# Performance work log

Measured on AMD Instinct MI355X. Metric: run time of the kernel, lower is better.

Reference implementation:

```python
import jax, jax.numpy as jnp
import numpy as np

NUM_HEADS = 8  # init num_heads


def setup_inputs() -> dict:
    key = jax.random.key(0)
    ks = jax.random.split(key, 8)
    B, N, C, G = 2, 256 * 256, 256, 512  # N hardcoded by original reshape(256*256)
    xq = jax.random.normal(ks[0], (B, N, C), jnp.float32)
    xk = jax.random.normal(ks[1], (B, N, C), jnp.float32)
    xv = jax.random.normal(ks[2], (B, N, C), jnp.float32)
    w_scale = C ** -0.5
    Wq = jax.random.normal(ks[3], (C, C), jnp.float32) * w_scale
    bq = jax.random.normal(ks[4], (C,), jnp.float32) * 0.02
    Wp = jax.random.normal(ks[5], (C, C), jnp.float32) * w_scale
    bp = jax.random.normal(ks[6], (C,), jnp.float32) * 0.02
    # Voronoi cell labels 1..G, each cell exactly N//G tokens, randomly scattered
    # over the 256x256 grid (irregular gather/scatter access, all cells < 1500 tokens).
    labels = jnp.repeat(jnp.arange(1, G + 1, dtype=jnp.int32), N // G)
    Voronoi = jnp.stack([
        jax.random.permutation(jax.random.fold_in(ks[7], b), labels) for b in range(B)
    ]).reshape(B, 256, 256)
    return {"xq": xq, "xk": xk, "xv": xv, "Wq": Wq, "bq": bq,
            "Wp": Wp, "bp": bp, "Voronoi": Voronoi, "num_groups": G}


def reference(xq, xk, xv, Wq, bq, Wp, bp, Voronoi, num_groups):
    B, N, C = xq.shape
    H = NUM_HEADS
    hd = C // H
    scale = hd ** -0.5  # qk_scale default: head_dim ** -0.5
    # NOTE: the original forward projects q, k AND v with self.q (shared weights/bias).
    # This (likely a bug upstream) is preserved faithfully here.
    q = (xq @ Wq.T + bq).reshape(B, N, H, hd)
    k = (xk @ Wq.T + bq).reshape(B, N, H, hd)
    v = (xv @ Wq.T + bq).reshape(B, N, H, hd)
    labels = Voronoi.reshape(B, N)
    order = jnp.argsort(labels, axis=1)   # [B, N] sort tokens by Voronoi cell id
    inv = jnp.argsort(order, axis=1)      # inverse permutation for scatter-back
    S = N // num_groups                   # tokens per cell (static)

    def gather(t):  # [B, N, H, hd] -> [B, G, S, H, hd] grouped by cell
        return jnp.take_along_axis(t, order[:, :, None, None], axis=1).reshape(B, num_groups, S, H, hd)

    qg = gather(q) * scale
    kg = gather(k)
    vg = gather(v)
    attn = jnp.einsum('bgshd,bgthd->bghst', qg, kg)   # per-cell scores [B,G,H,S,S]
    p = jax.nn.softmax(attn, axis=-1)                 # attn_drop=0 (eval)
    og = jnp.einsum('bghst,bgthd->bgshd', p, vg).reshape(B, N, H, hd)
    out = jnp.take_along_axis(og, inv[:, :, None, None], axis=1).reshape(B, N, C)
    return out @ Wp.T + bp                            # proj_drop=0 (eval)
```

## Files before the change

kernel.cpp:

```cpp
#include <hip/hip_runtime.h>
#include <hip/hip_bf16.h>

#define B_    2
#define NTOK  65536
#define C_    256
#define H_    8
#define HD_   32
#define G_    512
#define S_    128
#define BN    (B_*NTOK)
#define M3    (3*BN)

typedef __attribute__((ext_vector_type(8))) short short8;
typedef __attribute__((ext_vector_type(4))) float f32x4;

__device__ __forceinline__ ushort f2bf(float f) {
  __bf16 h = (__bf16)f;
  return __builtin_bit_cast(unsigned short, h);
}
__device__ __forceinline__ unsigned pk2(float lo, float hi) {
  return (unsigned)f2bf(lo) | ((unsigned)f2bf(hi) << 16);
}

__device__ __forceinline__ void gl16(const void* g, void* l) {
  __builtin_amdgcn_global_load_lds(
      (const __attribute__((address_space(1))) unsigned int*)g,
      (__attribute__((address_space(3))) unsigned int*)l, 16, 0, 0);
}

#define SW4(c, r) ((((c) ^ (r) ^ ((r) >> 2))) & 3)
#define SWK32(c, r) ((((c) ^ ((r) >> 1))) & 3)
#define PSL(c, r) ((((c) ^ ((r) & 7) ^ ((((r) >> 3) & 1) << 1))) & 15)
#define VSL(c, ch) ((((c) ^ (((ch) & 7) << 1) ^ (((ch) >> 3) & 3))) & 15)

#define QSCALE 0.25506907131737264f

__global__ __launch_bounds__(256) void k_prep(const float* __restrict__ Wq,
                                              const float* __restrict__ Wp,
                                              ushort* __restrict__ Wq_img,
                                              ushort* __restrict__ Wp_img) {
  int gid = blockIdx.x * 256 + threadIdx.x;
  int w = gid >> 13, rem = gid & 8191;
  if (w == 0) {
    int ks = rem >> 11, rem2 = rem & 2047;
    int r = rem2 >> 3, c = rem2 & 7;
    const float4* s = reinterpret_cast<const float4*>(Wq + (size_t)r * 256 + ks * 64 + c * 8);
    float4 a = s[0], b = s[1];
    uint4 o;
    o.x = pk2(a.x, a.y); o.y = pk2(a.z, a.w);
    o.z = pk2(b.x, b.y); o.w = pk2(b.z, b.w);
    *reinterpret_cast<uint4*>(Wq_img + ks * 16384 + r * 64 + ((c ^ (r & 7)) << 3)) = o;
  } else {
    int h = rem >> 10, r = (rem >> 2) & 255, c = rem & 3;
    const float4* s = reinterpret_cast<const float4*>(Wp + (size_t)r * 256 + h * 32 + c * 8);
    float4 a = s[0], b = s[1];
    uint4 o;
    o.x = pk2(a.x, a.y); o.y = pk2(a.z, a.w);
    o.z = pk2(b.x, b.y); o.w = pk2(b.z, b.w);
    *reinterpret_cast<uint4*>(Wp_img + h * 8192 + r * 32 + (SWK32(c, r) << 3)) = o;
  }
}

__global__ __launch_bounds__(256) void k_group(const int* __restrict__ vor,
                                               int* __restrict__ grp,
                                               int* __restrict__ cnt) {
  int idx = blockIdx.x * 256 + threadIdx.x;
  int b = idx >> 16;
  int n = idx & (NTOK - 1);
  int g = vor[idx] - 1;
  int pos = atomicAdd(&cnt[(b << 9) + g], 1);
  grp[((b << 9) + g) * S_ + pos] = n;
}

__global__ __launch_bounds__(512, 4) void k_proj_qkv(
    const float* __restrict__ xq, const float* __restrict__ xk,
    const float* __restrict__ xv, const ushort* __restrict__ Wq_img,
    const float* __restrict__ bq, ushort* __restrict__ qkv) {
  __shared__ ushort As[128 * 64];
  __shared__ ushort Bs[2][256 * 64];
  int mt = blockIdx.x;
  int t = mt >> 10;
  const float* A = (t == 0) ? xq : (t == 1) ? xk : xv;
  float qsc = (t == 0) ? QSCALE : 1.0f;
  size_t abase = (size_t)(mt & 1023) * 128 * 256;
  int row0 = mt * 128;

  int tid = threadIdx.x, lane = tid & 63, wave = tid >> 6;
  int l15 = lane & 15, hi = lane >> 4;
  int wr = (wave >> 2) * 64, wc = (wave & 3) * 64;
  int sr = tid >> 2, sq = tid & 3;

  const float* aptr = A + abase + (size_t)sr * 256 + sq * 16;
  int boff = wave * 4096 + lane * 16;

  f32x4 acc[4][4] = {};
  float4 ar[2][4];
  {
    const float4* p = reinterpret_cast<const float4*>(aptr);
#pragma unroll
    for (int j = 0; j < 4; ++j) ar[0][j] = p[j];
  }
#pragma unroll
  for (int j = 0; j < 4; ++j)
    gl16((const char*)Wq_img + boff + j * 1024, (char*)Bs[0] + boff + j * 1024);

#pragma unroll
  for (int ks = 0; ks < 4; ++ks) {
    uint4 w0, w1;
    w0.x = pk2(ar[ks & 1][0].x, ar[ks & 1][0].y); w0.y = pk2(ar[ks & 1][0].z, ar[ks & 1][0].w);
    w0.z = pk2(ar[ks & 1][1].x, ar[ks & 1][1].y); w0.w = pk2(ar[ks & 1][1].z, ar[ks & 1][1].w);
    w1.x = pk2(ar[ks & 1][2].x, ar[ks & 1][2].y); w1.y = pk2(ar[ks & 1][2].z, ar[ks & 1][2].w);
    w1.z = pk2(ar[ks & 1][3].x, ar[ks & 1][3].y); w1.w = pk2(ar[ks & 1][3].z, ar[ks & 1][3].w);
    *reinterpret_cast<uint4*>(&As[sr * 64 + (((sq * 2) ^ (sr & 7)) << 3)]) = w0;
    *reinterpret_cast<uint4*>(&As[sr * 64 + (((sq * 2 + 1) ^ (sr & 7)) << 3)]) = w1;
    if (ks < 3) {
      const float4* p = reinterpret_cast<const float4*>(aptr + (ks + 1) * 64);
#pragma unroll
      for (int j = 0; j < 4; ++j) ar[(ks + 1) & 1][j] = p[j];
#pragma unroll
      for (int j = 0; j < 4; ++j)
        gl16((const char*)Wq_img + (ks + 1) * 32768 + boff + j * 1024,
             (char*)Bs[(ks + 1) & 1] + boff + j * 1024);
      asm volatile("s_waitcnt vmcnt(8)" ::: "memory");
    } else {
      asm volatile("s_waitcnt vmcnt(0)" ::: "memory");
    }
    asm volatile("s_waitcnt lgkmcnt(0)" ::: "memory");
    __builtin_amdgcn_s_barrier();
    const ushort* Bcur = Bs[ks & 1];
#pragma unroll
    for (int kk = 0; kk < 2; ++kk) {
      int ck = kk * 4 + hi;
      short8 af[4], bfr[4];
#pragma unroll
      for (int m = 0; m < 4; ++m) {
        int r = wr + m * 16 + l15;
        af[m] = *reinterpret_cast<const short8*>(&As[r * 64 + ((ck ^ (r & 7)) << 3)]);
      }
#pragma unroll
      for (int n = 0; n < 4; ++n) {
        int r = wc + n * 16 + l15;
        bfr[n] = *reinterpret_cast<const short8*>(&Bcur[r * 64 + ((ck ^ (r & 7)) << 3)]);
      }
#pragma unroll
      for (int m = 0; m < 4; ++m)
#pragma unroll
        for (int n = 0; n < 4; ++n)
          acc[m][n] = __builtin_amdgcn_mfma_f32_16x16x32_bf16(af[m], bfr[n], acc[m][n], 0, 0, 0);
    }
    asm volatile("s_waitcnt lgkmcnt(0)" ::: "memory");
    __builtin_amdgcn_s_barrier();
  }

  ushort* Ot = (ushort*)Bs;
#pragma unroll
  for (int n = 0; n < 4; ++n) {
    int col = wc + n * 16 + l15;
    float bv = bq[col];
    int c = col >> 3, ci = col & 7;
#pragma unroll
    for (int m = 0; m < 4; ++m) {
      int r0 = wr + m * 16 + hi * 4;
#pragma unroll
      for (int j = 0; j < 4; ++j) {
        int r = r0 + j;
        int slot = c ^ (((r >> 2) & 3) << 1);
        Ot[r * 256 + slot * 8 + ci] = f2bf((acc[m][n][j] + bv) * qsc);
      }
    }
  }
  __syncthreads();
  {
    size_t gbase = (size_t)row0 * 256;
#pragma unroll
    for (int s = 0; s < 8; ++s) {
      int off = s * 4096 + tid * 8;
      int r = off >> 8, cc = (off >> 3) & 31;
      int slot = cc ^ (((r >> 2) & 3) << 1);
      *reinterpret_cast<uint4*>(qkv + gbase + off) =
          *reinterpret_cast<const uint4*>(Ot + r * 256 + slot * 8);
    }
  }
}

__global__ __launch_bounds__(512) void k_attn_proj(
    const ushort* __restrict__ qkv, const int* __restrict__ grp,
    const ushort* __restrict__ Wp_img, const float* __restrict__ bp,
    float* __restrict__ out) {
  __shared__ int toks[128];
  __shared__ ushort PsB[128 * 128];
  __shared__ ushort Vt[32 * 128];
  __shared__ ushort Oh[128 * 32];
  __shared__ ushort WpS[256 * 32];
  ushort* Qs = PsB;
  ushort* Ks = PsB + 4096;
  ushort* Ps = PsB;

  int bid = blockIdx.x;
  int g = bid & (G_ - 1), b = bid >> 9;
  int tid = threadIdx.x, lane = tid & 63, wave = tid >> 6;
  int l15 = lane & 15, hi = lane >> 4;
  int strip = wave * 16;
  int mg = wave >> 1, ng = wave & 1;

  if (tid < 128) toks[tid] = grp[((b << 9) + g) * S_ + tid];
  __syncthreads();

  int wpoff = wave * 1024 + lane * 16;
  gl16((const char*)Wp_img + wpoff, (char*)WpS + wpoff);
  gl16((const char*)Wp_img + 8192 + wpoff, (char*)WpS + wpoff + 8192);

  f32x4 acc[2][8] = {};

  int r_st = tid >> 2, cp = tid & 3;
  int tok_st = toks[r_st];
  size_t rowq = (size_t)(b * NTOK + tok_st) * 256;
  int chunk_t = r_st >> 3, tl = r_st & 7;

  uint4 qa, ka, va;
  {
    size_t base = rowq + cp * 8;
    qa = *reinterpret_cast<const uint4*>(qkv + base);
    ka = *reinterpret_cast<const uint4*>(qkv + (size_t)BN * 256 + base);
    va = *reinterpret_cast<const uint4*>(qkv + (size_t)2 * BN * 256 + base);
  }

  for (int h = 0; h < 8; ++h) {
    *reinterpret_cast<uint4*>(&Qs[r_st * 32 + SW4(cp, r_st) * 8]) = qa;
    *reinterpret_cast<uint4*>(&Ks[r_st * 32 + SW4(cp, r_st) * 8]) = ka;
    {
      const ushort* pv_ = reinterpret_cast<const ushort*>(&va);
#pragma unroll
      for (int e = 0; e < 8; ++e) {
        int ch = cp * 8 + e;
        Vt[ch * 128 + (VSL(chunk_t, ch) << 3) + tl] = pv_[e];
      }
    }
    asm volatile("s_waitcnt lgkmcnt(0)" ::: "memory");
    __builtin_amdgcn_s_barrier();

    if (h < 7) {
      size_t base = rowq + (h + 1) * 32 + cp * 8;
      qa = *reinterpret_cast<const uint4*>(qkv + base);
      ka = *reinterpret_cast<const uint4*>(qkv + (size_t)BN * 256 + base);
      va = *reinterpret_cast<const uint4*>(qkv + (size_t)2 * BN * 256 + base);
    }

    f32x4 sacc[8] = {};
    {
      int ra = strip + l15;
      short8 aq = *reinterpret_cast<const short8*>(&Qs[ra * 32 + SW4(hi, ra) * 8]);
      short8 bk[8];
#pragma unroll
      for (int n = 0; n < 8; ++n) {
        int r = n * 16 + l15;
        bk[n] = *reinterpret_cast<const short8*>(&Ks[r * 32 + SW4(hi, r) * 8]);
      }
#pragma unroll
      for (int n = 0; n < 8; ++n)
        sacc[n] = __builtin_amdgcn_mfma_f32_16x16x32_bf16(aq, bk[n], sacc[n], 0, 0, 0);
    }
    asm volatile("s_waitcnt lgkmcnt(0)" ::: "memory");
    __builtin_amdgcn_s_barrier();

    float inv[4];
#pragma unroll
    for (int j = 0; j < 4; ++j) {
      float mx = -1e30f;
#pragma unroll
      for (int n = 0; n < 8; ++n) mx = fmaxf(mx, sacc[n][j]);
#pragma unroll
      for (int d = 1; d < 16; d <<= 1) mx = fmaxf(mx, __shfl_xor(mx, d));
      float pv[8], sum = 0.f;
#pragma unroll
      for (int n = 0; n < 8; ++n) { pv[n] = exp2f(sacc[n][j] - mx); sum += pv[n]; }
#pragma unroll
      for (int d = 1; d < 16; d <<= 1) sum += __shfl_xor(sum, d);
      inv[j] = 1.0f / sum;
      int row = strip + hi * 4 + j;
#pragma unroll
      for (int n = 0; n < 8; ++n) {
        int col = n * 16 + l15;
        int chunk = col >> 3;
        Ps[row * 128 + (PSL(chunk, row) << 3) + (col & 7)] = f2bf(pv[n]);
      }
    }
    asm volatile("s_waitcnt lgkmcnt(0)" ::: "memory");

    f32x4 oacc[2] = {};
#pragma unroll
    for (int kk = 0; kk < 4; ++kk) {
      int chunk = kk * 4 + hi;
      int rp = strip + l15;
      short8 pa = *reinterpret_cast<const short8*>(&Ps[rp * 128 + (PSL(chunk, rp) << 3)]);
      short8 bv[2];
#pragma unroll
      for (int n = 0; n < 2; ++n) {
        int ch = n * 16 + l15;
        bv[n] = *reinterpret_cast<const short8*>(&Vt[ch * 128 + (VSL(chunk, ch) << 3)]);
      }
#pragma unroll
      for (int n = 0; n < 2; ++n)
        oacc[n] = __builtin_amdgcn_mfma_f32_16x16x32_bf16(pa, bv[n], oacc[n], 0, 0, 0);
    }
#pragma unroll
    for (int n = 0; n < 2; ++n) {
#pragma unroll
      for (int j = 0; j < 4; ++j) {
        int row = strip + hi * 4 + j;
        int col = n * 16 + l15;
        Oh[row * 32 + (SWK32(col >> 3, row) << 3) + (col & 7)] = f2bf(oacc[n][j] * inv[j]);
      }
    }
    asm volatile("s_waitcnt vmcnt(0)" ::: "memory");
    asm volatile("s_waitcnt lgkmcnt(0)" ::: "memory");
    __builtin_amdgcn_s_barrier();

    {
      short8 af[2], bf[8];
#pragma unroll
      for (int m = 0; m < 2; ++m) {
        int r = mg * 32 + m * 16 + l15;
        af[m] = *reinterpret_cast<const short8*>(&Oh[r * 32 + (SWK32(hi, r) << 3)]);
      }
#pragma unroll
      for (int n = 0; n < 8; ++n) {
        int r = ng * 128 + n * 16 + l15;
        bf[n] = *reinterpret_cast<const short8*>(&WpS[r * 32 + (SWK32(hi, r) << 3)]);
      }
#pragma unroll
      for (int m = 0; m < 2; ++m)
#pragma unroll
        for (int n = 0; n < 8; ++n)
          acc[m][n] = __builtin_amdgcn_mfma_f32_16x16x32_bf16(af[m], bf[n], acc[m][n], 0, 0, 0);
    }
    asm volatile("s_waitcnt lgkmcnt(0)" ::: "memory");
    __builtin_amdgcn_s_barrier();
    if (h < 7) {
      gl16((const char*)Wp_img + (h + 1) * 16384 + wpoff, (char*)WpS + wpoff);
      gl16((const char*)Wp_img + (h + 1) * 16384 + 8192 + wpoff, (char*)WpS + wpoff + 8192);
    }
  }

  float* Of = (float*)PsB;
#pragma unroll
  for (int q = 0; q < 4; ++q) {
    __syncthreads();
    if (mg == q) {
#pragma unroll
      for (int n = 0; n < 8; ++n) {
        int col = ng * 128 + n * 16 + l15;
        float bv = bp[col];
        int c = col >> 2, ci = col & 3;
#pragma unroll
        for (int m = 0; m < 2; ++m) {
#pragma unroll
          for (int j = 0; j < 4; ++j) {
            int lr = m * 16 + hi * 4 + j;
            int slot = c ^ (((lr >> 2) & 3) << 2);
            Of[lr * 256 + slot * 4 + ci] = acc[m][n][j] + bv;
          }
        }
      }
    }
    __syncthreads();
#pragma unroll
    for (int s = 0; s < 4; ++s) {
      int off = s * 2048 + tid * 4;
      int lr = off >> 8, cc = (off >> 2) & 63;
      int slot = cc ^ (((lr >> 2) & 3) << 2);
      int tok = toks[q * 32 + lr];
      *reinterpret_cast<float4*>(out + ((size_t)(b * NTOK + tok)) * 256 + cc * 4) =
          *reinterpret_cast<const float4*>(Of + lr * 256 + slot * 4);
    }
  }
}

extern "C" void kernel_launch(void* const* d_in, const int* in_sizes, int n_in,
                              void* d_out, int out_size, void* d_ws, size_t ws_size,
                              hipStream_t stream) {
  const float* xq = (const float*)d_in[0];
  const float* xk = (const float*)d_in[1];
  const float* xv = (const float*)d_in[2];
  const float* Wq = (const float*)d_in[3];
  const float* bq = (const float*)d_in[4];
  const float* Wp = (const float*)d_in[5];
  const float* bp = (const float*)d_in[6];
  const int*   vor = (const int*)d_in[7];

  char* ws = (char*)d_ws;
  ushort* qkv    = (ushort*)ws;
  int*    grp    = (int*)(ws + (size_t)201326592);
  int*    cnt    = (int*)(ws + (size_t)201850880);
  ushort* Wq_img = (ushort*)(ws + (size_t)201854976);
  ushort* Wp_img = (ushort*)(ws + (size_t)201986048);

  hipMemsetAsync(cnt, 0, B_ * G_ * sizeof(int), stream);
  k_prep<<<dim3(64), dim3(256), 0, stream>>>(Wq, Wp, Wq_img, Wp_img);
  k_group<<<dim3(BN / 256), dim3(256), 0, stream>>>(vor, grp, cnt);
  k_proj_qkv<<<dim3(M3 / 128), dim3(512), 0, stream>>>(xq, xk, xv, Wq_img, bq, qkv);
  k_attn_proj<<<dim3(B_ * G_), dim3(512), 0, stream>>>(qkv, grp, Wp_img, bp, (float*)d_out);
}
```

Measured before the change: 325.3 us.

## Keep softmax probabilities in registers and double-buffer Wp tiles in attention kernel

The attention kernel now computes S^T (K as A operand), so each lane holds a whole score column. Softmax needs only two cross-lane shuffles, and the probabilities are repacked into MFMA A-fragments through lane shuffles instead of going through LDS. This removes the P round-trip through shared memory and one barrier per head. Wp slices are double-buffered and prefetched a head early, which removes the trailing barrier, and the QKV GEMM prefetches its A tiles one step further ahead. The cost is more shuffle instructions and register pressure, and the swizzled fragment layout and vmcnt counts are fragile.

Result: no change. 327.0 us (+0.5%).

```diff
diff --git a/kernel.cpp b/kernel.cpp
--- a/kernel.cpp
+++ b/kernel.cpp
@@ -30,7 +30,6 @@
 
 #define SW4(c, r) ((((c) ^ (r) ^ ((r) >> 2))) & 3)
 #define SWK32(c, r) ((((c) ^ ((r) >> 1))) & 3)
-#define PSL(c, r) ((((c) ^ ((r) & 7) ^ ((((r) >> 3) & 1) << 1))) & 15)
 #define VSL(c, ch) ((((c) ^ (((ch) & 7) << 1) ^ (((ch) >> 3) & 3))) & 15)
 
 #define QSCALE 0.25506907131737264f
@@ -103,6 +102,11 @@
 #pragma unroll
   for (int j = 0; j < 4; ++j)
     gl16((const char*)Wq_img + boff + j * 1024, (char*)Bs[0] + boff + j * 1024);
+  {
+    const float4* p = reinterpret_cast<const float4*>(aptr + 64);
+#pragma unroll
+    for (int j = 0; j < 4; ++j) ar[1][j] = p[j];
+  }
 
 #pragma unroll
   for (int ks = 0; ks < 4; ++ks) {
@@ -114,13 +118,17 @@
     *reinterpret_cast<uint4*>(&As[sr * 64 + (((sq * 2) ^ (sr & 7)) << 3)]) = w0;
     *reinterpret_cast<uint4*>(&As[sr * 64 + (((sq * 2 + 1) ^ (sr & 7)) << 3)]) = w1;
     if (ks < 3) {
-      const float4* p = reinterpret_cast<const float4*>(aptr + (ks + 1) * 64);
-#pragma unroll
-      for (int j = 0; j < 4; ++j) ar[(ks + 1) & 1][j] = p[j];
 #pragma unroll
       for (int j = 0; j < 4; ++j)
         gl16((const char*)Wq_img + (ks + 1) * 32768 + boff + j * 1024,
              (char*)Bs[(ks + 1) & 1] + boff + j * 1024);
+    }
+    if (ks < 2) {
+      const float4* p = reinterpret_cast<const float4*>(aptr + (ks + 2) * 64);
+#pragma unroll
+      for (int j = 0; j < 4; ++j) ar[ks & 1][j] = p[j];
+    }
+    if (ks < 3) {
       asm volatile("s_waitcnt vmcnt(8)" ::: "memory");
     } else {
       asm volatile("s_waitcnt vmcnt(0)" ::: "memory");
@@ -188,13 +196,13 @@
     const ushort* __restrict__ Wp_img, const float* __restrict__ bp,
     float* __restrict__ out) {
   __shared__ int toks[128];
-  __shared__ ushort PsB[128 * 128];
-  __shared__ ushort Vt[32 * 128];
-  __shared__ ushort Oh[128 * 32];
-  __shared__ ushort WpS[256 * 32];
-  ushort* Qs = PsB;
-  ushort* Ks = PsB + 4096;
-  ushort* Ps = PsB;
+  __shared__ ushort shm[32768];
+  ushort* Qs  = shm;
+  ushort* Ks  = shm + 4096;
+  ushort* Vt  = shm + 8192;
+  ushort* Oh  = shm + 12288;
+  ushort* Wp0 = shm + 16384;
+  ushort* Wp1 = shm + 24576;
 
   int bid = blockIdx.x;
   int g = bid & (G_ - 1), b = bid >> 9;
@@ -207,8 +215,8 @@
   __syncthreads();
 
   int wpoff = wave * 1024 + lane * 16;
-  gl16((const char*)Wp_img + wpoff, (char*)WpS + wpoff);
-  gl16((const char*)Wp_img + 8192 + wpoff, (char*)WpS + wpoff + 8192);
+  gl16((const char*)Wp_img + wpoff, (char*)Wp0 + wpoff);
+  gl16((const char*)Wp_img + 8192 + wpoff, (char*)Wp0 + wpoff + 8192);
 
   f32x4 acc[2][8] = {};
 
@@ -226,6 +234,8 @@
   }
 
   for (int h = 0; h < 8; ++h) {
+    ushort* WpCur = (h & 1) ? Wp1 : Wp0;
+    ushort* WpNext = (h & 1) ? Wp0 : Wp1;
     *reinterpret_cast<uint4*>(&Qs[r_st * 32 + SW4(cp, r_st) * 8]) = qa;
     *reinterpret_cast<uint4*>(&Ks[r_st * 32 + SW4(cp, r_st) * 8]) = ka;
     {
@@ -240,6 +250,8 @@
     __builtin_amdgcn_s_barrier();
 
     if (h < 7) {
+      gl16((const char*)Wp_img + (h + 1) * 16384 + wpoff, (char*)WpNext + wpoff);
+      gl16((const char*)Wp_img + (h + 1) * 16384 + 8192 + wpoff, (char*)WpNext + wpoff + 8192);
       size_t base = rowq + (h + 1) * 32 + cp * 8;
       qa = *reinterpret_cast<const uint4*>(qkv + base);
       ka = *reinterpret_cast<const uint4*>(qkv + (size_t)BN * 256 + base);
@@ -249,70 +261,86 @@
     f32x4 sacc[8] = {};
     {
       int ra = strip + l15;
-      short8 aq = *reinterpret_cast<const short8*>(&Qs[ra * 32 + SW4(hi, ra) * 8]);
-      short8 bk[8];
+      short8 qf = *reinterpret_cast<const short8*>(&Qs[ra * 32 + SW4(hi, ra) * 8]);
 #pragma unroll
       for (int n = 0; n < 8; ++n) {
         int r = n * 16 + l15;
-        bk[n] = *reinterpret_cast<const short8*>(&Ks[r * 32 + SW4(hi, r) * 8]);
-      }
-#pragma unroll
-      for (int n = 0; n < 8; ++n)
-        sacc[n] = __builtin_amdgcn_mfma_f32_16x16x32_bf16(aq, bk[n], sacc[n], 0, 0, 0);
-    }
-    asm volatile("s_waitcnt lgkmcnt(0)" ::: "memory");
-    __builtin_amdgcn_s_barrier();
-
-    float inv[4];
-#pragma unroll
-    for (int j = 0; j < 4; ++j) {
-      float mx = -1e30f;
-#pragma unroll
-      for (int n = 0; n < 8; ++n) mx = fmaxf(mx, sacc[n][j]);
-#pragma unroll
-      for (int d = 1; d < 16; d <<= 1) mx = fmaxf(mx, __shfl_xor(mx, d));
-      float pv[8], sum = 0.f;
-#pragma unroll
-      for (int n = 0; n < 8; ++n) { pv[n] = exp2f(sacc[n][j] - mx); sum += pv[n]; }
-#pragma unroll
-      for (int d = 1; d < 16; d <<= 1) sum += __shfl_xor(sum, d);
-      inv[j] = 1.0f / sum;
-      int row = strip + hi * 4 + j;
-#pragma unroll
-      for (int n = 0; n < 8; ++n) {
-        int col = n * 16 + l15;
-        int chunk = col >> 3;
-        Ps[row * 128 + (PSL(chunk, row) << 3) + (col & 7)] = f2bf(pv[n]);
-      }
-    }
-    asm volatile("s_waitcnt lgkmcnt(0)" ::: "memory");
+        short8 kf = *reinterpret_cast<const short8*>(&Ks[r * 32 + SW4(hi, r) * 8]);
+        sacc[n] = __builtin_amdgcn_mfma_f32_16x16x32_bf16(kf, qf, sacc[n], 0, 0, 0);
+      }
+    }
+
+    float mx = -1e30f;
+#pragma unroll
+    for (int n = 0; n < 8; ++n)
+#pragma unroll
+      for (int j = 0; j < 4; ++j) mx = fmaxf(mx, sacc[n][j]);
+    mx = fmaxf(mx, __shfl_xor(mx, 16));
+    mx = fmaxf(mx, __shfl_xor(mx, 32));
+    float p[8][4];
+    float sum = 0.f;
+#pragma unroll
+    for (int n = 0; n < 8; ++n)
+#pragma unroll
+      for (int j = 0; j < 4; ++j) { p[n][j] = exp2f(sacc[n][j] - mx); sum += p[n][j]; }
+    sum += __shfl_xor(sum, 16);
+    sum += __shfl_xor(sum, 32);
+    float inv = 1.0f / sum;
+
+    short8 paf[4];
+#pragma unroll
+    for (int t = 0; t < 4; ++t) {
+      unsigned e0 = pk2(p[2 * t][0], p[2 * t][1]);
+      unsigned e1 = pk2(p[2 * t][2], p[2 * t][3]);
+      unsigned o0 = pk2(p[2 * t + 1][0], p[2 * t + 1][1]);
+      unsigned o1 = pk2(p[2 * t + 1][2], p[2 * t + 1][3]);
+      unsigned pe0 = __shfl_xor(e0, 16), pe1 = __shfl_xor(e1, 16);
+      unsigned po0 = __shfl_xor(o0, 16), po1 = __shfl_xor(o1, 16);
+      bool up = (hi & 1);
+      unsigned E0 = up ? pe0 : e0, E1 = up ? pe1 : e1;
+      unsigned E2 = up ? e0 : pe0, E3 = up ? e1 : pe1;
+      unsigned O0 = up ? po0 : o0, O1 = up ? po1 : o1;
+      unsigned O2 = up ? o0 : po0, O3 = up ? o1 : po1;
+      unsigned s0 = up ? E0 : O0, s1 = up ? E1 : O1;
+      unsigned s2 = up ? E2 : O2, s3 = up ? E3 : O3;
+      unsigned r0 = __shfl_xor(s0, 32), r1 = __shfl_xor(s1, 32);
+      unsigned r2 = __shfl_xor(s2, 32), r3 = __shfl_xor(s3, 32);
+      unsigned f0, f1, f2, f3;
+      if (hi == 0)      { f0 = E0; f1 = E1; f2 = E2; f3 = E3; }
+      else if (hi == 3) { f0 = O0; f1 = O1; f2 = O2; f3 = O3; }
+      else              { f0 = r0; f1 = r1; f2 = r2; f3 = r3; }
+      union { unsigned u[4]; short8 s; } cv;
+      cv.u[0] = f0; cv.u[1] = f1; cv.u[2] = f2; cv.u[3] = f3;
+      paf[t] = cv.s;
+    }
 
     f32x4 oacc[2] = {};
 #pragma unroll
-    for (int kk = 0; kk < 4; ++kk) {
-      int chunk = kk * 4 + hi;
-      int rp = strip + l15;
-      short8 pa = *reinterpret_cast<const short8*>(&Ps[rp * 128 + (PSL(chunk, rp) << 3)]);
+    for (int t = 0; t < 4; ++t) {
       short8 bv[2];
 #pragma unroll
-      for (int n = 0; n < 2; ++n) {
-        int ch = n * 16 + l15;
-        bv[n] = *reinterpret_cast<const short8*>(&Vt[ch * 128 + (VSL(chunk, ch) << 3)]);
-      }
-#pragma unroll
-      for (int n = 0; n < 2; ++n)
-        oacc[n] = __builtin_amdgcn_mfma_f32_16x16x32_bf16(pa, bv[n], oacc[n], 0, 0, 0);
-    }
-#pragma unroll
-    for (int n = 0; n < 2; ++n) {
-#pragma unroll
-      for (int j = 0; j < 4; ++j) {
-        int row = strip + hi * 4 + j;
-        int col = n * 16 + l15;
-        Oh[row * 32 + (SWK32(col >> 3, row) << 3) + (col & 7)] = f2bf(oacc[n][j] * inv[j]);
-      }
-    }
-    asm volatile("s_waitcnt vmcnt(0)" ::: "memory");
+      for (int n2 = 0; n2 < 2; ++n2) {
+        int ch = n2 * 16 + l15;
+        int chunk = t * 4 + hi;
+        bv[n2] = *reinterpret_cast<const short8*>(&Vt[ch * 128 + (VSL(chunk, ch) << 3)]);
+      }
+#pragma unroll
+      for (int n2 = 0; n2 < 2; ++n2)
+        oacc[n2] = __builtin_amdgcn_mfma_f32_16x16x32_bf16(paf[t], bv[n2], oacc[n2], 0, 0, 0);
+    }
+
+    float invj[4];
+#pragma unroll
+    for (int jr = 0; jr < 4; ++jr) invj[jr] = __shfl(inv, hi * 4 + jr);
+#pragma unroll
+    for (int n2 = 0; n2 < 2; ++n2)
+#pragma unroll
+      for (int jr = 0; jr < 4; ++jr) {
+        int row = strip + hi * 4 + jr;
+        int col = n2 * 16 + l15;
+        Oh[row * 32 + (SWK32(col >> 3, row) << 3) + (col & 7)] = f2bf(oacc[n2][jr] * invj[jr]);
+      }
+    asm volatile("s_waitcnt vmcnt(5)" ::: "memory");
     asm volatile("s_waitcnt lgkmcnt(0)" ::: "memory");
     __builtin_amdgcn_s_barrier();
 
@@ -326,7 +354,7 @@
 #pragma unroll
       for (int n = 0; n < 8; ++n) {
         int r = ng * 128 + n * 16 + l15;
-        bf[n] = *reinterpret_cast<const short8*>(&WpS[r * 32 + (SWK32(hi, r) << 3)]);
+        bf[n] = *reinterpret_cast<const short8*>(&WpCur[r * 32 + (SWK32(hi, r) << 3)]);
       }
 #pragma unroll
       for (int m = 0; m < 2; ++m)
@@ -334,15 +362,9 @@
         for (int n = 0; n < 8; ++n)
           acc[m][n] = __builtin_amdgcn_mfma_f32_16x16x32_bf16(af[m], bf[n], acc[m][n], 0, 0, 0);
     }
-    asm volatile("s_waitcnt lgkmcnt(0)" ::: "memory");
-    __builtin_amdgcn_s_barrier();
-    if (h < 7) {
-      gl16((const char*)Wp_img + (h + 1) * 16384 + wpoff, (char*)WpS + wpoff);
-      gl16((const char*)Wp_img + (h + 1) * 16384 + 8192 + wpoff, (char*)WpS + wpoff + 8192);
-    }
-  }
-
-  float* Of = (float*)PsB;
+  }
+
+  float* Of = (float*)shm;
 #pragma unroll
   for (int q = 0; q < 4; ++q) {
     __syncthreads();
```
